# Kernel optimization log

Measured on AMD Instinct MI355X. Metric: run time of the kernel, lower is better.

The kernel has to match this reference:

```python
import jax, jax.numpy as jnp
import numpy as np

NUM_HEADS = 12
LOCAL_WINDOW = 7


def setup_inputs() -> dict:
    key = jax.random.key(0)
    k1, k2, k3 = jax.random.split(key, 3)
    B, N, C = 2, 2048, 768
    x = jax.random.normal(k1, (B, N, C), dtype=jnp.float32)
    w_qkv = jax.random.normal(k2, (3 * C, C), dtype=jnp.float32) * (C ** -0.5)
    w_proj = jax.random.normal(k3, (C, C), dtype=jnp.float32) * (C ** -0.5)
    b_proj = jnp.zeros((C,), dtype=jnp.float32)
    return {"x": x, "w_qkv": w_qkv, "w_proj": w_proj, "b_proj": b_proj}


def reference(x, w_qkv, w_proj, b_proj):
    B, N, C = x.shape
    H = NUM_HEADS
    Dh = C // H
    scale = Dh ** -0.5
    # local-window additive mask: 0 within |i-j|<=w, -inf outside (vectorized)
    idx = jnp.arange(N)
    local_mask = jnp.where(
        jnp.abs(idx[:, None] - idx[None, :]) <= LOCAL_WINDOW, 0.0, -jnp.inf
    ).astype(x.dtype)
    qkv = x @ w_qkv.T
    qkv = qkv.reshape(B, N, 3, H, Dh).transpose(2, 0, 3, 1, 4)
    q, k, v = qkv[0], qkv[1], qkv[2]
    attn = jnp.einsum("bhnd,bhmd->bhnm", q, k) * scale
    attn = attn + local_mask[None, None, :, :]
    attn = jax.nn.softmax(attn, axis=-1)
    out = jnp.einsum("bhnm,bhmd->bhnd", attn, v)
    out = out.transpose(0, 2, 1, 3).reshape(B, N, C)
    return out @ w_proj.T + b_proj
```

## Files before the change

### kernel.cpp

```cpp
#include <hip/hip_runtime.h>
#include <hip/hip_bf16.h>

typedef __bf16 bf16;
typedef bf16 bf16x4 __attribute__((ext_vector_type(4)));
typedef bf16 bf16x8 __attribute__((ext_vector_type(8)));
typedef float floatx4 __attribute__((ext_vector_type(4)));

#define GLOBAL_AS __attribute__((address_space(1)))
#define LDS_AS __attribute__((address_space(3)))

__global__ __launch_bounds__(256)
void cvt3_f32_bf16(const float* __restrict__ s0, const float* __restrict__ s1,
                   const float* __restrict__ s2, bf16* __restrict__ d0,
                   bf16* __restrict__ d1, bf16* __restrict__ d2,
                   int n0, int n1, int n2)
{
    int t = blockIdx.x * blockDim.x + threadIdx.x;
    const float* s; bf16* d; int i;
    if (t < n0)                { s = s0; d = d0; i = t; }
    else if (t < n0 + n1)      { s = s1; d = d1; i = t - n0; }
    else if (t < n0 + n1 + n2) { s = s2; d = d2; i = t - n0 - n1; }
    else return;
    float4 v = ((const float4*)s)[i];
    bf16x4 o = { (bf16)v.x, (bf16)v.y, (bf16)v.z, (bf16)v.w };
    ((bf16x4*)d)[i] = o;
}

template<typename CT, bool AF32, bool WF32, int M, int N, int K, int LDA, int LDC>
__global__ __launch_bounds__(256, 2)
void gemm_bt(const void* __restrict__ Av, const void* __restrict__ Wv,
             CT* __restrict__ C, const float* __restrict__ bias)
{
    __shared__ __align__(16) bf16 As[128 * 32];
    __shared__ __align__(16) bf16 Bs[128 * 32];

    const int tid  = threadIdx.x;
    const int lane = tid & 63;
    const int wave = tid >> 6;
    const int row0 = blockIdx.x * 128;
    const int col0 = blockIdx.y * 128;

    const int wm = (wave & 1) * 64;
    const int wn = (wave >> 1) * 64;

    floatx4 acc[4][4] = {};

    const int fr = lane & 15;
    const int fk = (lane >> 4) * 8;

    const int lr = lane >> 2;
    const int lk = (lane & 3) * 8;

    for (int k0 = 0; k0 < K; k0 += 32) {
        if (!AF32 && !WF32) {
            #pragma unroll
            for (int c = 0; c < 2; ++c) {
                const int chunk = wave * 2 + c;
                const int r = chunk * 16 + lr;
                const bf16* gA = (const bf16*)Av + (size_t)(row0 + r) * LDA + k0 + lk;
                const bf16* gB = (const bf16*)Wv + (size_t)(col0 + r) * K + k0 + lk;
                __builtin_amdgcn_global_load_lds((const GLOBAL_AS void*)gA,
                                                 (LDS_AS void*)(As + chunk * 512),
                                                 16, 0, 0);
                __builtin_amdgcn_global_load_lds((const GLOBAL_AS void*)gB,
                                                 (LDS_AS void*)(Bs + chunk * 512),
                                                 16, 0, 0);
            }
        } else {
            #pragma unroll
            for (int c = 0; c < 2; ++c) {
                const int idx = tid + c * 256;
                const int r   = idx >> 2;
                const int cb  = (idx & 3) * 8;

                bf16x8 va, vw;
                if (AF32) {
                    const float4* g = (const float4*)((const float*)Av
                                       + (size_t)(row0 + r) * LDA + k0 + cb);
                    float4 g0 = g[0], g1 = g[1];
                    va[0]=(bf16)g0.x; va[1]=(bf16)g0.y; va[2]=(bf16)g0.z; va[3]=(bf16)g0.w;
                    va[4]=(bf16)g1.x; va[5]=(bf16)g1.y; va[6]=(bf16)g1.z; va[7]=(bf16)g1.w;
                } else {
                    va = *(const bf16x8*)((const bf16*)Av
                                       + (size_t)(row0 + r) * LDA + k0 + cb);
                }
                if (WF32) {
                    const float4* g = (const float4*)((const float*)Wv
                                       + (size_t)(col0 + r) * K + k0 + cb);
                    float4 g0 = g[0], g1 = g[1];
                    vw[0]=(bf16)g0.x; vw[1]=(bf16)g0.y; vw[2]=(bf16)g0.z; vw[3]=(bf16)g0.w;
                    vw[4]=(bf16)g1.x; vw[5]=(bf16)g1.y; vw[6]=(bf16)g1.z; vw[7]=(bf16)g1.w;
                } else {
                    vw = *(const bf16x8*)((const bf16*)Wv
                                       + (size_t)(col0 + r) * K + k0 + cb);
                }
                *(bf16x8*)(As + r * 32 + cb) = va;
                *(bf16x8*)(Bs + r * 32 + cb) = vw;
            }
        }
        __syncthreads();

        bf16x8 af[4], bfr[4];
        #pragma unroll
        for (int i = 0; i < 4; ++i) {
            af[i]  = *(const bf16x8*)(As + (wm + i * 16 + fr) * 32 + fk);
            bfr[i] = *(const bf16x8*)(Bs + (wn + i * 16 + fr) * 32 + fk);
        }
        #pragma unroll
        for (int i = 0; i < 4; ++i)
            #pragma unroll
            for (int j = 0; j < 4; ++j)
                acc[i][j] = __builtin_amdgcn_mfma_f32_16x16x32_bf16(
                    af[i], bfr[j], acc[i][j], 0, 0, 0);

        __syncthreads();
    }

    const int fc  = lane & 15;
    const int fr4 = (lane >> 4) * 4;
    #pragma unroll
    for (int i = 0; i < 4; ++i) {
        #pragma unroll
        for (int j = 0; j < 4; ++j) {
            const int col = col0 + wn + j * 16 + fc;
            const float b = bias ? bias[col] : 0.0f;
            #pragma unroll
            for (int r = 0; r < 4; ++r) {
                const int row = row0 + wm + i * 16 + fr4 + r;
                C[(size_t)row * LDC + col] = (CT)(acc[i][j][r] + b);
            }
        }
    }
}

__global__ __launch_bounds__(256)
void attn_tile(bf16* __restrict__ qkv)
{
    __shared__ __align__(16) bf16 Ks[4][32][72];
    __shared__ __align__(16) bf16 Vt[4][64][40];
    __shared__ __align__(16) bf16 Ps[4][16][40];

    const int w    = threadIdx.x >> 6;
    const int lane = threadIdx.x & 63;
    const int c    = lane & 15;
    const int q    = lane >> 4;
    const int wid  = blockIdx.x * 4 + w;
    const int it   = wid & 127;
    const int bh   = wid >> 7;
    const int h    = bh % 12;
    const int b    = bh / 12;
    const int I0   = it * 16;
    const int bbase = b * 2048;
    const int j0   = I0 - 7;

    #pragma unroll
    for (int itr = 0; itr < 4; ++itr) {
        int idx = itr * 64 + lane;
        int row = idx >> 3;
        int dc  = (idx & 7) * 8;
        int jc  = j0 + row; jc = jc < 0 ? 0 : (jc > 2047 ? 2047 : jc);
        const bf16* base = qkv + (size_t)(bbase + jc) * 2304 + h * 64 + dc;
        bf16x8 kv = *(const bf16x8*)(base + 768);
        bf16x8 vv = *(const bf16x8*)(base + 1536);
        *(bf16x8*)(&Ks[w][row][dc]) = kv;
        #pragma unroll
        for (int e = 0; e < 8; ++e) Vt[w][dc + e][row] = vv[e];
    }

    const bf16* qrow = qkv + (size_t)(bbase + I0 + c) * 2304 + h * 64;
    bf16x8 aq0 = *(const bf16x8*)(qrow + q * 8);
    bf16x8 aq1 = *(const bf16x8*)(qrow + 32 + q * 8);

    __syncthreads();

    floatx4 st[2] = {};
    #pragma unroll
    for (int t = 0; t < 2; ++t) {
        bf16x8 k0 = *(const bf16x8*)(&Ks[w][t * 16 + c][q * 8]);
        bf16x8 k1 = *(const bf16x8*)(&Ks[w][t * 16 + c][32 + q * 8]);
        st[t] = __builtin_amdgcn_mfma_f32_16x16x32_bf16(aq0, k0, st[t], 0, 0, 0);
        st[t] = __builtin_amdgcn_mfma_f32_16x16x32_bf16(aq1, k1, st[t], 0, 0, 0);
    }

    float s[2][4];
    #pragma unroll
    for (int t = 0; t < 2; ++t)
        #pragma unroll
        for (int r = 0; r < 4; ++r) {
            int il = q * 4 + r;
            int jl = t * 16 + c;
            int ja = j0 + jl;
            bool valid = (jl >= il) && (jl <= il + 14) && (ja >= 0) && (ja < 2048);
            s[t][r] = valid ? st[t][r] * 0.125f : -1e30f;
        }

    float mx[4], l[4], p[2][4];
    #pragma unroll
    for (int r = 0; r < 4; ++r) {
        float m2 = fmaxf(s[0][r], s[1][r]);
        #pragma unroll
        for (int mk = 1; mk < 16; mk <<= 1) m2 = fmaxf(m2, __shfl_xor(m2, mk, 64));
        mx[r] = m2;
        p[0][r] = __expf(s[0][r] - m2);
        p[1][r] = __expf(s[1][r] - m2);
        float l2 = p[0][r] + p[1][r];
        #pragma unroll
        for (int mk = 1; mk < 16; mk <<= 1) l2 += __shfl_xor(l2, mk, 64);
        l[r] = l2;
    }

    #pragma unroll
    for (int r = 0; r < 4; ++r) {
        Ps[w][q * 4 + r][c]      = (bf16)p[0][r];
        Ps[w][q * 4 + r][16 + c] = (bf16)p[1][r];
    }
    __syncthreads();

    bf16x8 ap = *(const bf16x8*)(&Ps[w][c][q * 8]);
    floatx4 ov[4];
    #pragma unroll
    for (int nt = 0; nt < 4; ++nt) {
        bf16x8 vf = *(const bf16x8*)(&Vt[w][nt * 16 + c][q * 8]);
        floatx4 z = {};
        ov[nt] = __builtin_amdgcn_mfma_f32_16x16x32_bf16(ap, vf, z, 0, 0, 0);
    }

    float rl[4];
    #pragma unroll
    for (int r = 0; r < 4; ++r) rl[r] = 1.0f / l[r];
    #pragma unroll
    for (int r = 0; r < 4; ++r) {
        bf16* orow = qkv + (size_t)(bbase + I0 + q * 4 + r) * 2304 + h * 64;
        #pragma unroll
        for (int nt = 0; nt < 4; ++nt)
            orow[nt * 16 + c] = (bf16)(ov[nt][r] * rl[r]);
    }
}

extern "C" void kernel_launch(void* const* d_in, const int* in_sizes, int n_in,
                              void* d_out, int out_size, void* d_ws, size_t ws_size,
                              hipStream_t stream)
{
    const float* x      = (const float*)d_in[0];
    const float* w_qkv  = (const float*)d_in[1];
    const float* w_proj = (const float*)d_in[2];
    const float* b_proj = (const float*)d_in[3];
    float* out = (float*)d_out;

    bf16* qkv = (bf16*)d_ws;
    const size_t QKV_B  = (size_t)4096 * 2304 * 2;
    const size_t XB_B   = (size_t)4096 * 768 * 2;
    const size_t WQKV_B = (size_t)2304 * 768 * 2;
    const size_t WPRJ_B = (size_t)768 * 768 * 2;

    if (ws_size >= QKV_B + XB_B + WQKV_B + WPRJ_B) {
        bf16* xb  = (bf16*)((char*)d_ws + QKV_B);
        bf16* wqb = (bf16*)((char*)xb + XB_B);
        bf16* wpb = (bf16*)((char*)wqb + WQKV_B);

        const int n0 = 4096 * 768 / 4, n1 = 2304 * 768 / 4, n2 = 768 * 768 / 4;
        cvt3_f32_bf16<<<dim3((n0 + n1 + n2) / 256), 256, 0, stream>>>(
            x, w_qkv, w_proj, xb, wqb, wpb, n0, n1, n2);

        gemm_bt<bf16, false, false, 4096, 2304, 768, 768, 2304>
            <<<dim3(32, 18), 256, 0, stream>>>(xb, wqb, qkv, nullptr);

        attn_tile<<<dim3(768), 256, 0, stream>>>(qkv);

        gemm_bt<float, false, false, 4096, 768, 768, 2304, 768>
            <<<dim3(32, 6), 256, 0, stream>>>(qkv, wpb, out, b_proj);
    } else {
        gemm_bt<bf16, true, true, 4096, 2304, 768, 768, 2304>
            <<<dim3(32, 18), 256, 0, stream>>>(x, w_qkv, qkv, nullptr);

        attn_tile<<<dim3(768), 256, 0, stream>>>(qkv);

        gemm_bt<float, false, true, 4096, 768, 768, 2304, 768>
            <<<dim3(32, 6), 256, 0, stream>>>(qkv, w_proj, out, b_proj);
    }
}
```

Baseline: 126.6 us.

## Fuse fp32-to-bf16 conversion into GEMM loads and write attention output to compact buffer

```diff
diff --git a/kernel.cpp b/kernel.cpp
--- a/kernel.cpp
+++ b/kernel.cpp
@@ -2,29 +2,11 @@
 #include <hip/hip_bf16.h>
 
 typedef __bf16 bf16;
-typedef bf16 bf16x4 __attribute__((ext_vector_type(4)));
 typedef bf16 bf16x8 __attribute__((ext_vector_type(8)));
 typedef float floatx4 __attribute__((ext_vector_type(4)));
 
 #define GLOBAL_AS __attribute__((address_space(1)))
 #define LDS_AS __attribute__((address_space(3)))
-
-__global__ __launch_bounds__(256)
-void cvt3_f32_bf16(const float* __restrict__ s0, const float* __restrict__ s1,
-                   const float* __restrict__ s2, bf16* __restrict__ d0,
-                   bf16* __restrict__ d1, bf16* __restrict__ d2,
-                   int n0, int n1, int n2)
-{
-    int t = blockIdx.x * blockDim.x + threadIdx.x;
-    const float* s; bf16* d; int i;
-    if (t < n0)                { s = s0; d = d0; i = t; }
-    else if (t < n0 + n1)      { s = s1; d = d1; i = t - n0; }
-    else if (t < n0 + n1 + n2) { s = s2; d = d2; i = t - n0 - n1; }
-    else return;
-    float4 v = ((const float4*)s)[i];
-    bf16x4 o = { (bf16)v.x, (bf16)v.y, (bf16)v.z, (bf16)v.w };
-    ((bf16x4*)d)[i] = o;
-}
 
 template<typename CT, bool AF32, bool WF32, int M, int N, int K, int LDA, int LDC>
 __global__ __launch_bounds__(256, 2)
@@ -52,50 +34,54 @@
     const int lk = (lane & 3) * 8;
 
     for (int k0 = 0; k0 < K; k0 += 32) {
-        if (!AF32 && !WF32) {
+        if (AF32) {
+            #pragma unroll
+            for (int c = 0; c < 2; ++c) {
+                const int idx = tid + c * 256;
+                const int r   = idx >> 2;
+                const int cb  = (idx & 3) * 8;
+                const float4* g = (const float4*)((const float*)Av
+                                   + (size_t)(row0 + r) * LDA + k0 + cb);
+                float4 g0 = g[0], g1 = g[1];
+                bf16x8 va;
+                va[0]=(bf16)g0.x; va[1]=(bf16)g0.y; va[2]=(bf16)g0.z; va[3]=(bf16)g0.w;
+                va[4]=(bf16)g1.x; va[5]=(bf16)g1.y; va[6]=(bf16)g1.z; va[7]=(bf16)g1.w;
+                *(bf16x8*)(As + r * 32 + cb) = va;
+            }
+        } else {
             #pragma unroll
             for (int c = 0; c < 2; ++c) {
                 const int chunk = wave * 2 + c;
                 const int r = chunk * 16 + lr;
                 const bf16* gA = (const bf16*)Av + (size_t)(row0 + r) * LDA + k0 + lk;
-                const bf16* gB = (const bf16*)Wv + (size_t)(col0 + r) * K + k0 + lk;
                 __builtin_amdgcn_global_load_lds((const GLOBAL_AS void*)gA,
                                                  (LDS_AS void*)(As + chunk * 512),
                                                  16, 0, 0);
-                __builtin_amdgcn_global_load_lds((const GLOBAL_AS void*)gB,
-                                                 (LDS_AS void*)(Bs + chunk * 512),
-                                                 16, 0, 0);
-            }
-        } else {
+            }
+        }
+        if (WF32) {
             #pragma unroll
             for (int c = 0; c < 2; ++c) {
                 const int idx = tid + c * 256;
                 const int r   = idx >> 2;
                 const int cb  = (idx & 3) * 8;
-
-                bf16x8 va, vw;
-                if (AF32) {
-                    const float4* g = (const float4*)((const float*)Av
-                                       + (size_t)(row0 + r) * LDA + k0 + cb);
-                    float4 g0 = g[0], g1 = g[1];
-                    va[0]=(bf16)g0.x; va[1]=(bf16)g0.y; va[2]=(bf16)g0.z; va[3]=(bf16)g0.w;
-                    va[4]=(bf16)g1.x; va[5]=(bf16)g1.y; va[6]=(bf16)g1.z; va[7]=(bf16)g1.w;
-                } else {
-                    va = *(const bf16x8*)((const bf16*)Av
-                                       + (size_t)(row0 + r) * LDA + k0 + cb);
-                }
-                if (WF32) {
-                    const float4* g = (const float4*)((const float*)Wv
-                                       + (size_t)(col0 + r) * K + k0 + cb);
-                    float4 g0 = g[0], g1 = g[1];
-                    vw[0]=(bf16)g0.x; vw[1]=(bf16)g0.y; vw[2]=(bf16)g0.z; vw[3]=(bf16)g0.w;
-                    vw[4]=(bf16)g1.x; vw[5]=(bf16)g1.y; vw[6]=(bf16)g1.z; vw[7]=(bf16)g1.w;
-                } else {
-                    vw = *(const bf16x8*)((const bf16*)Wv
-                                       + (size_t)(col0 + r) * K + k0 + cb);
-                }
-                *(bf16x8*)(As + r * 32 + cb) = va;
+                const float4* g = (const float4*)((const float*)Wv
+                                   + (size_t)(col0 + r) * K + k0 + cb);
+                float4 g0 = g[0], g1 = g[1];
+                bf16x8 vw;
+                vw[0]=(bf16)g0.x; vw[1]=(bf16)g0.y; vw[2]=(bf16)g0.z; vw[3]=(bf16)g0.w;
+                vw[4]=(bf16)g1.x; vw[5]=(bf16)g1.y; vw[6]=(bf16)g1.z; vw[7]=(bf16)g1.w;
                 *(bf16x8*)(Bs + r * 32 + cb) = vw;
+            }
+        } else {
+            #pragma unroll
+            for (int c = 0; c < 2; ++c) {
+                const int chunk = wave * 2 + c;
+                const int r = chunk * 16 + lr;
+                const bf16* gB = (const bf16*)Wv + (size_t)(col0 + r) * K + k0 + lk;
+                __builtin_amdgcn_global_load_lds((const GLOBAL_AS void*)gB,
+                                                 (LDS_AS void*)(Bs + chunk * 512),
+                                                 16, 0, 0);
             }
         }
         __syncthreads();
@@ -134,7 +120,7 @@
 }
 
 __global__ __launch_bounds__(256)
-void attn_tile(bf16* __restrict__ qkv)
+void attn_tile(const bf16* __restrict__ qkv, bf16* __restrict__ aout)
 {
     __shared__ __align__(16) bf16 Ks[4][32][72];
     __shared__ __align__(16) bf16 Vt[4][64][40];
@@ -194,13 +180,12 @@
             s[t][r] = valid ? st[t][r] * 0.125f : -1e30f;
         }
 
-    float mx[4], l[4], p[2][4];
+    float l[4], p[2][4];
     #pragma unroll
     for (int r = 0; r < 4; ++r) {
         float m2 = fmaxf(s[0][r], s[1][r]);
         #pragma unroll
         for (int mk = 1; mk < 16; mk <<= 1) m2 = fmaxf(m2, __shfl_xor(m2, mk, 64));
-        mx[r] = m2;
         p[0][r] = __expf(s[0][r] - m2);
         p[1][r] = __expf(s[1][r] - m2);
         float l2 = p[0][r] + p[1][r];
@@ -230,7 +215,110 @@
     for (int r = 0; r < 4; ++r) rl[r] = 1.0f / l[r];
     #pragma unroll
     for (int r = 0; r < 4; ++r) {
-        bf16* orow = qkv + (size_t)(bbase + I0 + q * 4 + r) * 2304 + h * 64;
+        bf16* orow = aout + (size_t)(bbase + I0 + q * 4 + r) * 768 + h * 64;
+        #pragma unroll
+        for (int nt = 0; nt < 4; ++nt)
+            orow[nt * 16 + c] = (bf16)(ov[nt][r] * rl[r]);
+    }
+}
+
+__global__ __launch_bounds__(256)
+void attn_tile_ip(bf16* __restrict__ qkv)
+{
+    __shared__ __align__(16) bf16 Ks[4][32][72];
+    __shared__ __align__(16) bf16 Vt[4][64][40];
+    __shared__ __align__(16) bf16 Ps[4][16][40];
+
+    const int w    = threadIdx.x >> 6;
+    const int lane = threadIdx.x & 63;
+    const int c    = lane & 15;
+    const int q    = lane >> 4;
+    const int wid  = blockIdx.x * 4 + w;
+    const int it   = wid & 127;
+    const int bh   = wid >> 7;
+    const int h    = bh % 12;
+    const int b    = bh / 12;
+    const int I0   = it * 16;
+    const int bbase = b * 2048;
+    const int j0   = I0 - 7;
+
+    #pragma unroll
+    for (int itr = 0; itr < 4; ++itr) {
+        int idx = itr * 64 + lane;
+        int row = idx >> 3;
+        int dc  = (idx & 7) * 8;
+        int jc  = j0 + row; jc = jc < 0 ? 0 : (jc > 2047 ? 2047 : jc);
+        const bf16* base = qkv + (size_t)(bbase + jc) * 2304 + h * 64 + dc;
+        bf16x8 kv = *(const bf16x8*)(base + 768);
+        bf16x8 vv = *(const bf16x8*)(base + 1536);
+        *(bf16x8*)(&Ks[w][row][dc]) = kv;
+        #pragma unroll
+        for (int e = 0; e < 8; ++e) Vt[w][dc + e][row] = vv[e];
+    }
+
+    const bf16* qrow = qkv + (size_t)(bbase + I0 + c) * 2304 + h * 64;
+    bf16x8 aq0 = *(const bf16x8*)(qrow + q * 8);
+    bf16x8 aq1 = *(const bf16x8*)(qrow + 32 + q * 8);
+
+    __syncthreads();
+
+    floatx4 st[2] = {};
+    #pragma unroll
+    for (int t = 0; t < 2; ++t) {
+        bf16x8 k0 = *(const bf16x8*)(&Ks[w][t * 16 + c][q * 8]);
+        bf16x8 k1 = *(const bf16x8*)(&Ks[w][t * 16 + c][32 + q * 8]);
+        st[t] = __builtin_amdgcn_mfma_f32_16x16x32_bf16(aq0, k0, st[t], 0, 0, 0);
+        st[t] = __builtin_amdgcn_mfma_f32_16x16x32_bf16(aq1, k1, st[t], 0, 0, 0);
+    }
+
+    float s[2][4];
+    #pragma unroll
+    for (int t = 0; t < 2; ++t)
+        #pragma unroll
+        for (int r = 0; r < 4; ++r) {
+            int il = q * 4 + r;
+            int jl = t * 16 + c;
+            int ja = j0 + jl;
+            bool valid = (jl >= il) && (jl <= il + 14) && (ja >= 0) && (ja < 2048);
+            s[t][r] = valid ? st[t][r] * 0.125f : -1e30f;
+        }
+
+    float l[4], p[2][4];
+    #pragma unroll
+    for (int r = 0; r < 4; ++r) {
+        float m2 = fmaxf(s[0][r], s[1][r]);
+        #pragma unroll
+        for (int mk = 1; mk < 16; mk <<= 1) m2 = fmaxf(m2, __shfl_xor(m2, mk, 64));
+        p[0][r] = __expf(s[0][r] - m2);
+        p[1][r] = __expf(s[1][r] - m2);
+        float l2 = p[0][r] + p[1][r];
+        #pragma unroll
+        for (int mk = 1; mk < 16; mk <<= 1) l2 += __shfl_xor(l2, mk, 64);
+        l[r] = l2;
+    }
+
+    #pragma unroll
+    for (int r = 0; r < 4; ++r) {
+        Ps[w][q * 4 + r][c]      = (bf16)p[0][r];
+        Ps[w][q * 4 + r][16 + c] = (bf16)p[1][r];
+    }
+    __syncthreads();
+
+    bf16x8 ap = *(const bf16x8*)(&Ps[w][c][q * 8]);
+    floatx4 ov[4];
+    #pragma unroll
+    for (int nt = 0; nt < 4; ++nt) {
+        bf16x8 vf = *(const bf16x8*)(&Vt[w][nt * 16 + c][q * 8]);
+        floatx4 z = {};
+        ov[nt] = __builtin_amdgcn_mfma_f32_16x16x32_bf16(ap, vf, z, 0, 0, 0);
+    }
+
+    float rl[4];
+    #pragma unroll
+    for (int r = 0; r < 4; ++r) rl[r] = 1.0f / l[r];
+    #pragma unroll
+    for (int r = 0; r < 4; ++r) {
+        bf16* orow = (bf16*)qkv + (size_t)(bbase + I0 + q * 4 + r) * 2304 + h * 64;
         #pragma unroll
         for (int nt = 0; nt < 4; ++nt)
             orow[nt * 16 + c] = (bf16)(ov[nt][r] * rl[r]);
@@ -248,33 +336,21 @@
     float* out = (float*)d_out;
 
     bf16* qkv = (bf16*)d_ws;
-    const size_t QKV_B  = (size_t)4096 * 2304 * 2;
-    const size_t XB_B   = (size_t)4096 * 768 * 2;
-    const size_t WQKV_B = (size_t)2304 * 768 * 2;
-    const size_t WPRJ_B = (size_t)768 * 768 * 2;
-
-    if (ws_size >= QKV_B + XB_B + WQKV_B + WPRJ_B) {
-        bf16* xb  = (bf16*)((char*)d_ws + QKV_B);
-        bf16* wqb = (bf16*)((char*)xb + XB_B);
-        bf16* wpb = (bf16*)((char*)wqb + WQKV_B);
-
-        const int n0 = 4096 * 768 / 4, n1 = 2304 * 768 / 4, n2 = 768 * 768 / 4;
-        cvt3_f32_bf16<<<dim3((n0 + n1 + n2) / 256), 256, 0, stream>>>(
-            x, w_qkv, w_proj, xb, wqb, wpb, n0, n1, n2);
-
-        gemm_bt<bf16, false, false, 4096, 2304, 768, 768, 2304>
-            <<<dim3(32, 18), 256, 0, stream>>>(xb, wqb, qkv, nullptr);
-
-        attn_tile<<<dim3(768), 256, 0, stream>>>(qkv);
-
-        gemm_bt<float, false, false, 4096, 768, 768, 2304, 768>
-            <<<dim3(32, 6), 256, 0, stream>>>(qkv, wpb, out, b_proj);
+    const size_t QKV_B = (size_t)4096 * 2304 * 2;
+    const size_t AO_B  = (size_t)4096 * 768 * 2;
+
+    gemm_bt<bf16, true, true, 4096, 2304, 768, 768, 2304>
+        <<<dim3(32, 18), 256, 0, stream>>>(x, w_qkv, qkv, nullptr);
+
+    if (ws_size >= QKV_B + AO_B) {
+        bf16* aout = (bf16*)((char*)d_ws + QKV_B);
+
+        attn_tile<<<dim3(768), 256, 0, stream>>>(qkv, aout);
+
+        gemm_bt<float, false, true, 4096, 768, 768, 768, 768>
+            <<<dim3(32, 6), 256, 0, stream>>>(aout, w_proj, out, b_proj);
     } else {
-        gemm_bt<bf16, true, true, 4096, 2304, 768, 768, 2304>
-            <<<dim3(32, 18), 256, 0, stream>>>(x, w_qkv, qkv, nullptr);
-
-        attn_tile<<<dim3(768), 256, 0, stream>>>(qkv);
-
+        attn_tile_ip<<<dim3(768), 256, 0, stream>>>(qkv);
         gemm_bt<float, false, true, 4096, 768, 768, 2304, 768>
             <<<dim3(32, 6), 256, 0, stream>>>(qkv, w_proj, out, b_proj);
     }
```

Result: slower. 136.5 us (+7.8%).
